# Performance work log

Hardware: AMD Instinct MI355X
Metric: run time of the kernel (lower is better)

Reference implementation:

```python
import jax, jax.numpy as jnp
import numpy as np
from jax import lax

B, N = 8, 4096
NPOINT, RADIUS, NSAMPLE = 1024, 0.2, 32
MLP = [64, 64, 128]
FEAT = 64
ALPHA = 0.2          # LeakyReLU slope
BN_EPS = 1e-5        # BatchNorm eps (eval mode, running_mean=0, running_var=1)
BIG = 1e10


def setup_inputs() -> dict:
    key = jax.random.key(0)
    ks = jax.random.split(key, 16)
    xyz = jax.random.uniform(ks[0], (B, N, 3), dtype=jnp.float32)
    feats = jax.random.normal(ks[1], (B, N, FEAT), dtype=jnp.float32)
    d = {"points": jnp.concatenate([xyz, feats], axis=-1)}
    ch = [FEAT] + MLP
    for i in range(len(MLP)):
        d[f"W{i}"] = jax.random.normal(ks[2 + 3 * i], (ch[i + 1], ch[i]), dtype=jnp.float32) * 0.1
        d[f"b{i}"] = jnp.zeros((ch[i + 1],), jnp.float32)
        d[f"g{i}"] = jnp.ones((ch[i + 1],), jnp.float32)
        d[f"be{i}"] = jnp.zeros((ch[i + 1],), jnp.float32)
    d["a_att"] = jax.random.uniform(ks[12], (3 + MLP[-1], MLP[-1]), jnp.float32, -0.3, 0.3)
    return d


def _gather(points, idx):
    # points: [B, N, D], idx: [B, ...] -> [B, ..., D]
    return jax.vmap(lambda p, i: p[i])(points, idx)


def farthest_point_sample(xyz, npoint):
    # xyz: [B, N, 3] -> [B, npoint] (deterministic start at index 0)
    b, n, _ = xyz.shape
    def step(carry, _):
        distance, farthest = carry
        centered = jnp.take_along_axis(xyz, farthest[:, None, None], axis=1)  # [B,1,3]
        dist = jnp.sum((xyz - centered) ** 2, axis=-1)                        # [B,N]
        distance = jnp.minimum(distance, dist)
        return (distance, jnp.argmax(distance, axis=-1)), farthest
    init = (jnp.full((b, n), BIG, dtype=xyz.dtype), jnp.zeros((b,), dtype=jnp.int32))
    _, idxs = lax.scan(step, init, None, length=npoint)
    return jnp.transpose(idxs)  # [B, npoint]


def query_ball_point(nsample, radius, xyz, centered_xyz):
    # squared distances [B, npoint, N]
    d = (-2.0 * jnp.einsum('bpc,bnc->bpn', centered_xyz, xyz)
         + jnp.sum(centered_xyz ** 2, -1)[..., None]
         + jnp.sum(xyz ** 2, -1)[:, None, :])
    d = jnp.where(d > radius ** 2, BIG, d)
    order = jnp.argsort(d, axis=-1)[..., :nsample]                    # [B,np,ns]
    sv = jnp.take_along_axis(d, order, axis=-1)                       # sorted values
    first = order[..., 0:1]
    return jnp.where(sv == BIG, first, order)


def _mlp(x, params):
    # x: [..., C]; 1x1 conv + BN(eval, mean=0, var=1) + relu per layer
    for (W, b, g, be) in params:
        x = jnp.einsum('...c,oc->...o', x, W) + b
        x = x * (g / jnp.sqrt(1.0 + BN_EPS)) + be
        x = jax.nn.relu(x)
    return x


def reference(points, W0, b0, g0, be0, W1, b1, g1, be1, W2, b2, g2, be2, a_att):
    xyz = points[..., :3]
    feats = points[..., 3:]
    cidx = farthest_point_sample(xyz, NPOINT)          # [B, npoint]
    cxyz = _gather(xyz, cidx)                          # [B, npoint, 3]
    cfeat = _gather(feats, cidx)                       # [B, npoint, D]
    gidx = query_ball_point(NSAMPLE, RADIUS, xyz, cxyz)  # [B, npoint, nsample]
    gxyz = _gather(xyz, gidx)                          # [B, npoint, ns, 3]
    gfeat = _gather(feats, gidx)                       # [B, npoint, ns, D]

    params = [(W0, b0, g0, be0), (W1, b1, g1, be1), (W2, b2, g2, be2)]
    cfeat = _mlp(cfeat, params)                        # [B, npoint, D']
    gfeat = _mlp(gfeat, params)                        # [B, npoint, ns, D']

    cpts = jnp.concatenate([cxyz, cfeat], axis=-1)     # [B, npoint, 3+D']
    gpts = jnp.concatenate([gxyz, gfeat], axis=-1)     # [B, npoint, ns, 3+D']

    delta = gpts - cpts[:, :, None, :]
    att = jax.nn.leaky_relu(jnp.einsum('bpnc,cd->bpnd', delta, a_att), ALPHA)
    att = jax.nn.softmax(att, axis=2)                  # over nsample (eval: no dropout)
    gac = jnp.sum(att * gfeat, axis=2)                 # [B, npoint, D']
    return jnp.concatenate([cxyz, gac], axis=-1)       # [B, npoint, 3+D']
```

## Files before the change

### kernel.cpp

```cpp
#include <hip/hip_runtime.h>
#include <math.h>

#define NBATCH 8
#define NPTS 4096
#define NPOINT 1024
#define NSAMPLE 32
#define PTDIM 67
#define BIGF 1e10f

#define DPP_QUAD_XOR1 0xB1
#define DPP_QUAD_XOR2 0x4E
#define DPP_ROW_HALF_MIRROR 0x141
#define DPP_ROW_MIRROR 0x140
#define DPP_ROW_BCAST15 0x142
#define DPP_ROW_BCAST31 0x143

template <int CTRL>
__device__ inline float dpp_mov_f(float v) {
  int i = __float_as_int(v);
  return __int_as_float(__builtin_amdgcn_update_dpp(i, i, CTRL, 0xf, 0xf, false));
}
template <int CTRL>
__device__ inline unsigned dpp_mov_u(unsigned v) {
  return (unsigned)__builtin_amdgcn_update_dpp((int)v, (int)v, CTRL, 0xf, 0xf, false);
}
template <int CTRL>
__device__ inline void dpp_min2(unsigned& hi, unsigned& lo) {
  unsigned nh = dpp_mov_u<CTRL>(hi);
  unsigned nl = dpp_mov_u<CTRL>(lo);
  bool take = (nh < hi) || (nh == hi && nl < lo);
  hi = take ? nh : hi;
  lo = take ? nl : lo;
}
__device__ inline unsigned fmap(float d) {
  unsigned b = __float_as_uint(d);
  return ((int)b < 0) ? ~b : (b | 0x80000000u);
}
#define FMAP_INF 0xFF800000u

__device__ inline float red32_max(float v) {
  v = fmaxf(v, dpp_mov_f<DPP_QUAD_XOR1>(v));
  v = fmaxf(v, dpp_mov_f<DPP_QUAD_XOR2>(v));
  v = fmaxf(v, dpp_mov_f<DPP_ROW_HALF_MIRROR>(v));
  v = fmaxf(v, dpp_mov_f<DPP_ROW_MIRROR>(v));
  v = fmaxf(v, __shfl_xor(v, 16));
  return v;
}
__device__ inline float red32_sum(float v) {
  v += dpp_mov_f<DPP_QUAD_XOR1>(v);
  v += dpp_mov_f<DPP_QUAD_XOR2>(v);
  v += dpp_mov_f<DPP_ROW_HALF_MIRROR>(v);
  v += dpp_mov_f<DPP_ROW_MIRROR>(v);
  v += __shfl_xor(v, 16);
  return v;
}

struct FpsS {
  unsigned long long slots[2][4];
  int cidxS[NPOINT];
  float4 C[NPTS];
};
struct MlpS {
  float w0[64 * 64], w1[64 * 64], w2[128 * 64];
  float bb0[64], ss0[64], ee0[64];
  float bb1[64], ss1[64], ee1[64];
  float bb2[128], ss2[128], ee2[128];
};
#define F1_SMEM (sizeof(MlpS) > sizeof(FpsS) ? sizeof(MlpS) : sizeof(FpsS))

__device__ void fps_body(char* smemRaw, const float* __restrict__ pts,
                         int* __restrict__ cidx, float* __restrict__ X,
                         float* __restrict__ Y, float* __restrict__ Z) {
#pragma clang fp contract(off)
  FpsS* S = (FpsS*)smemRaw;
  const int b = blockIdx.x, tid = threadIdx.x;
  const int w = tid >> 6, lane = tid & 63;
  const float* pb = pts + (size_t)b * NPTS * PTDIM;
  float2 px2[8], py2[8], pz2[8];
  float dl[16];
  #pragma unroll
  for (int k = 0; k < 16; k++) {
    int j = tid + (k << 8);
    const float* pj = pb + (size_t)j * PTDIM;
    float x = pj[0], y = pj[1], z = pj[2];
    if (k & 1) { px2[k >> 1].y = x; py2[k >> 1].y = y; pz2[k >> 1].y = z; }
    else       { px2[k >> 1].x = x; py2[k >> 1].x = y; pz2[k >> 1].x = z; }
    S->C[j] = make_float4(x, y, z, 0.0f);
    X[b * NPTS + j] = x; Y[b * NPTS + j] = y; Z[b * NPTS + j] = z;
    dl[k] = BIGF;
  }
  __syncthreads();
  int f = 0;
  float4 c0 = S->C[0];
  float cx = c0.x, cy = c0.y, cz = c0.z;
  for (int t = 0; t < NPOINT; t++) {
    if (tid == 0) S->cidxS[t] = f;
    float2 c2x = make_float2(cx, cx);
    float2 c2y = make_float2(cy, cy);
    float2 c2z = make_float2(cz, cz);
    #pragma unroll
    for (int m = 0; m < 8; m++) {
      float2 dx = px2[m] - c2x;
      float2 dy = py2[m] - c2y;
      float2 dz = pz2[m] - c2z;
      float2 d = (dx * dx + dy * dy) + dz * dz;
      dl[2 * m]     = fminf(dl[2 * m],     d.x);
      dl[2 * m + 1] = fminf(dl[2 * m + 1], d.y);
    }
    float u0 = fmaxf(dl[0], dl[1]),  u1 = fmaxf(dl[2], dl[3]);
    float u2 = fmaxf(dl[4], dl[5]),  u3 = fmaxf(dl[6], dl[7]);
    float u4 = fmaxf(dl[8], dl[9]),  u5 = fmaxf(dl[10], dl[11]);
    float u6 = fmaxf(dl[12], dl[13]), u7 = fmaxf(dl[14], dl[15]);
    float v0 = fmaxf(u0, u1), v1 = fmaxf(u2, u3);
    float v2 = fmaxf(u4, u5), v3 = fmaxf(u6, u7);
    float bv = fmaxf(fmaxf(v0, v1), fmaxf(v2, v3));
    float m = bv;
    m = fmaxf(m, dpp_mov_f<DPP_QUAD_XOR1>(m));
    m = fmaxf(m, dpp_mov_f<DPP_QUAD_XOR2>(m));
    m = fmaxf(m, dpp_mov_f<DPP_ROW_HALF_MIRROR>(m));
    m = fmaxf(m, dpp_mov_f<DPP_ROW_MIRROR>(m));
    m = fmaxf(m, dpp_mov_f<DPP_ROW_BCAST15>(m));
    m = fmaxf(m, dpp_mov_f<DPP_ROW_BCAST31>(m));
    unsigned wmaxbits = (unsigned)__builtin_amdgcn_readlane(__float_as_int(m), 63);
    unsigned c_[16];
    #pragma unroll
    for (int k = 0; k < 16; k++)
      c_[k] = (__float_as_uint(dl[k]) == wmaxbits) ? (unsigned)(tid + (k << 8)) : 0xFFFFFFFFu;
    unsigned q0 = min(c_[0], c_[1]),  q1 = min(c_[2], c_[3]);
    unsigned q2 = min(c_[4], c_[5]),  q3 = min(c_[6], c_[7]);
    unsigned q4 = min(c_[8], c_[9]),  q5 = min(c_[10], c_[11]);
    unsigned q6 = min(c_[12], c_[13]), q7 = min(c_[14], c_[15]);
    unsigned r0 = min(q0, q1), r1 = min(q2, q3), r2 = min(q4, q5), r3 = min(q6, q7);
    unsigned cand = min(min(r0, r1), min(r2, r3));
    cand = min(cand, dpp_mov_u<DPP_QUAD_XOR1>(cand));
    cand = min(cand, dpp_mov_u<DPP_QUAD_XOR2>(cand));
    cand = min(cand, dpp_mov_u<DPP_ROW_HALF_MIRROR>(cand));
    cand = min(cand, dpp_mov_u<DPP_ROW_MIRROR>(cand));
    cand = min(cand, dpp_mov_u<DPP_ROW_BCAST15>(cand));
    cand = min(cand, dpp_mov_u<DPP_ROW_BCAST31>(cand));
    unsigned jmin = (unsigned)__builtin_amdgcn_readlane((int)cand, 63);
    if (lane == 0)
      S->slots[t & 1][w] = ((unsigned long long)wmaxbits << 32) |
                           (unsigned long long)(NPTS - 1 - jmin);
    __syncthreads();
    unsigned long long s0 = S->slots[t & 1][0], s1 = S->slots[t & 1][1];
    unsigned long long s2 = S->slots[t & 1][2], s3 = S->slots[t & 1][3];
    unsigned long long m0 = s0 > s1 ? s0 : s1;
    unsigned long long m1 = s2 > s3 ? s2 : s3;
    unsigned long long best = m0 > m1 ? m0 : m1;
    f = NPTS - 1 - (int)(best & 0xFFFFFFFFull);
    float4 cc = S->C[f];
    cx = cc.x; cy = cc.y; cz = cc.z;
  }
  __syncthreads();
  for (int i = tid; i < NPOINT; i += 256) cidx[b * NPOINT + i] = S->cidxS[i];
}

__device__ void mlp_body(char* smemRaw, const float* __restrict__ pts,
    const float* __restrict__ W0, const float* __restrict__ B0, const float* __restrict__ G0, const float* __restrict__ E0,
    const float* __restrict__ W1, const float* __restrict__ B1, const float* __restrict__ G1, const float* __restrict__ E1,
    const float* __restrict__ W2, const float* __restrict__ B2, const float* __restrict__ G2, const float* __restrict__ E2,
    float* __restrict__ mfeat) {
  MlpS* S = (MlpS*)smemRaw;
  const float INVS = 0.99999500003750f;
  const int t = threadIdx.x;
  for (int i = t; i < 4096; i += 256) { S->w0[i] = W0[i]; S->w1[i] = W1[i]; }
  for (int i = t; i < 8192; i += 256) { S->w2[i] = W2[i]; }
  if (t < 64) {
    S->bb0[t] = B0[t]; S->ss0[t] = G0[t] * INVS; S->ee0[t] = E0[t];
    S->bb1[t] = B1[t]; S->ss1[t] = G1[t] * INVS; S->ee1[t] = E1[t];
  }
  if (t < 128) { S->bb2[t] = B2[t]; S->ss2[t] = G2[t] * INVS; S->ee2[t] = E2[t]; }
  __syncthreads();

  const size_t r = (size_t)(blockIdx.x - 8) * 256 + t;
  const float* xr = pts + r * PTDIM + 3;
  float x[64];
  #pragma unroll
  for (int c = 0; c < 64; c++) x[c] = xr[c];

  float h1[64];
  #pragma unroll
  for (int o = 0; o < 64; o++) {
    float acc = S->bb0[o];
    #pragma unroll
    for (int c = 0; c < 64; c += 4) {
      float4 wv = *(const float4*)&S->w0[o * 64 + c];
      acc = fmaf(wv.x, x[c], acc);
      acc = fmaf(wv.y, x[c + 1], acc);
      acc = fmaf(wv.z, x[c + 2], acc);
      acc = fmaf(wv.w, x[c + 3], acc);
    }
    h1[o] = fmaxf(fmaf(acc, S->ss0[o], S->ee0[o]), 0.0f);
  }
  float h2[64];
  #pragma unroll
  for (int o = 0; o < 64; o++) {
    float acc = S->bb1[o];
    #pragma unroll
    for (int c = 0; c < 64; c += 4) {
      float4 wv = *(const float4*)&S->w1[o * 64 + c];
      acc = fmaf(wv.x, h1[c], acc);
      acc = fmaf(wv.y, h1[c + 1], acc);
      acc = fmaf(wv.z, h1[c + 2], acc);
      acc = fmaf(wv.w, h1[c + 3], acc);
    }
    h2[o] = fmaxf(fmaf(acc, S->ss1[o], S->ee1[o]), 0.0f);
  }
  float* orow = mfeat + r * 128;
  #pragma unroll
  for (int o = 0; o < 128; o += 4) {
    float a0 = S->bb2[o], a1 = S->bb2[o + 1], a2 = S->bb2[o + 2], a3 = S->bb2[o + 3];
    #pragma unroll
    for (int c = 0; c < 64; c += 4) {
      float4 wv0 = *(const float4*)&S->w2[(o    ) * 64 + c];
      float4 wv1 = *(const float4*)&S->w2[(o + 1) * 64 + c];
      float4 wv2 = *(const float4*)&S->w2[(o + 2) * 64 + c];
      float4 wv3 = *(const float4*)&S->w2[(o + 3) * 64 + c];
      a0 = fmaf(wv0.x, h2[c], a0); a0 = fmaf(wv0.y, h2[c+1], a0); a0 = fmaf(wv0.z, h2[c+2], a0); a0 = fmaf(wv0.w, h2[c+3], a0);
      a1 = fmaf(wv1.x, h2[c], a1); a1 = fmaf(wv1.y, h2[c+1], a1); a1 = fmaf(wv1.z, h2[c+2], a1); a1 = fmaf(wv1.w, h2[c+3], a1);
      a2 = fmaf(wv2.x, h2[c], a2); a2 = fmaf(wv2.y, h2[c+1], a2); a2 = fmaf(wv2.z, h2[c+2], a2); a2 = fmaf(wv2.w, h2[c+3], a2);
      a3 = fmaf(wv3.x, h2[c], a3); a3 = fmaf(wv3.y, h2[c+1], a3); a3 = fmaf(wv3.z, h2[c+2], a3); a3 = fmaf(wv3.w, h2[c+3], a3);
    }
    float4 ov;
    ov.x = fmaxf(fmaf(a0, S->ss2[o    ], S->ee2[o    ]), 0.0f);
    ov.y = fmaxf(fmaf(a1, S->ss2[o + 1], S->ee2[o + 1]), 0.0f);
    ov.z = fmaxf(fmaf(a2, S->ss2[o + 2], S->ee2[o + 2]), 0.0f);
    ov.w = fmaxf(fmaf(a3, S->ss2[o + 3], S->ee2[o + 3]), 0.0f);
    *(float4*)(orow + o) = ov;
  }
}

__global__ __launch_bounds__(256) void f1_kernel(const float* __restrict__ pts,
    const float* __restrict__ W0, const float* __restrict__ B0, const float* __restrict__ G0, const float* __restrict__ E0,
    const float* __restrict__ W1, const float* __restrict__ B1, const float* __restrict__ G1, const float* __restrict__ E1,
    const float* __restrict__ W2, const float* __restrict__ B2, const float* __restrict__ G2, const float* __restrict__ E2,
    float* __restrict__ mfeat, int* __restrict__ cidx,
    float* __restrict__ X, float* __restrict__ Y, float* __restrict__ Z) {
  __shared__ __align__(16) char smem[F1_SMEM];
  if (blockIdx.x < 8)
    fps_body(smem, pts, cidx, X, Y, Z);
  else
    mlp_body(smem, pts, W0, B0, G0, E0, W1, B1, G1, E1, W2, B2, G2, E2, mfeat);
}

#define F2_SMEM 16768

__device__ void ballq_body(char* smemRaw,
                           const float* __restrict__ X, const float* __restrict__ Y,
                           const float* __restrict__ Z, const int* __restrict__ cidx,
                           int* __restrict__ gidx) {
  float (*dbuf)[512] = (float (*)[512])smemRaw;
  int   (*ibuf)[512] = (int (*)[512])(smemRaw + 4 * 512 * 4);
  const int t = threadIdx.x;
  const int w = t >> 6, lane = t & 63;
  const int pc = blockIdx.x * 4 + w;
  const int b = pc >> 10;
  const float* Xb = X + b * NPTS;
  const float* Yb = Y + b * NPTS;
  const float* Zb = Z + b * NPTS;
  const int cI = cidx[pc];
  const float cx = Xb[cI], cy = Yb[cI], cz = Zb[cI];
  const float sc = __fadd_rn(__fadd_rn(__fmul_rn(cx, cx), __fmul_rn(cy, cy)), __fmul_rn(cz, cz));
  const float R2 = 0.04f;
  int cnt = 0;
  for (int rr = 0; rr < 16; rr++) {
    const int base = rr * 256 + lane * 4;
    float4 px4 = *(const float4*)(Xb + base);
    float4 py4 = *(const float4*)(Yb + base);
    float4 pz4 = *(const float4*)(Zb + base);
    #pragma unroll
    for (int e = 0; e < 4; e++) {
      float px = e == 0 ? px4.x : e == 1 ? px4.y : e == 2 ? px4.z : px4.w;
      float py = e == 0 ? py4.x : e == 1 ? py4.y : e == 2 ? py4.z : py4.w;
      float pz = e == 0 ? pz4.x : e == 1 ? pz4.y : e == 2 ? pz4.z : pz4.w;
      float dot = __fadd_rn(__fadd_rn(__fmul_rn(cx, px), __fmul_rn(cy, py)), __fmul_rn(cz, pz));
      float sx  = __fadd_rn(__fadd_rn(__fmul_rn(px, px), __fmul_rn(py, py)), __fmul_rn(pz, pz));
      float d   = __fadd_rn(__fadd_rn(__fmul_rn(-2.0f, dot), sc), sx);
      bool pred = !(d > R2);
      unsigned long long mask = __ballot(pred);
      if (pred) {
        int pos = cnt + (int)__popcll(mask & ((1ull << lane) - 1ull));
        if (pos < 512) { dbuf[w][pos] = d; ibuf[w][pos] = base + e; }
      }
      cnt += (int)__popcll(mask);
    }
  }
  const int K = cnt < 512 ? cnt : 512;
  unsigned long long kk[8];
  #pragma unroll
  for (int k = 0; k < 8; k++) {
    int pos = lane + 64 * k;
    if (pos < K)
      kk[k] = ((unsigned long long)fmap(dbuf[w][pos]) << 32) | (unsigned)ibuf[w][pos];
    else
      kk[k] = ((unsigned long long)FMAP_INF << 32) | 0x7fffffffu;
  }
  int first = 0;
  int* gout = gidx + pc * NSAMPLE;
  for (int it = 0; it < NSAMPLE; it++) {
    unsigned long long best = kk[0];
    #pragma unroll
    for (int k = 1; k < 8; k++) if (kk[k] < best) best = kk[k];
    unsigned hi = (unsigned)(best >> 32), lo = (unsigned)best;
    dpp_min2<DPP_QUAD_XOR1>(hi, lo);
    dpp_min2<DPP_QUAD_XOR2>(hi, lo);
    dpp_min2<DPP_ROW_HALF_MIRROR>(hi, lo);
    dpp_min2<DPP_ROW_MIRROR>(hi, lo);
    dpp_min2<DPP_ROW_BCAST15>(hi, lo);
    dpp_min2<DPP_ROW_BCAST31>(hi, lo);
    unsigned blo = (unsigned)__builtin_amdgcn_readlane((int)lo, 63);
    #pragma unroll
    for (int k = 0; k < 8; k++)
      if ((unsigned)kk[k] == blo)
        kk[k] = (kk[k] & 0xFFFFFFFFull) | ((unsigned long long)FMAP_INF << 32);
    if (it == 0) first = (int)blo;
    if (lane == 0) gout[it] = (it < K) ? (int)blo : first;
  }
}

__device__ void proj_body(char* smemRaw,
                          const float* __restrict__ X, const float* __restrict__ Y,
                          const float* __restrict__ Z, const float* __restrict__ mfeat,
                          const float* __restrict__ Aatt, float* __restrict__ P) {
  float* As = (float*)smemRaw;
  const int t = threadIdx.x;
  const int pb = blockIdx.x - 2048;
  const int grp = pb & 3;
  const int tile = pb >> 2;
  for (int i = t; i < 131 * 32; i += 256) {
    int c = i >> 5, col = i & 31;
    As[i] = Aatt[c * 128 + grp * 32 + col];
  }
  __syncthreads();
  const int r0 = tile * 512 + t * 2;
  float acc0[32], acc1[32];
  {
    float x0 = X[r0], y0 = Y[r0], z0 = Z[r0];
    float x1 = X[r0 + 1], y1 = Y[r0 + 1], z1 = Z[r0 + 1];
    #pragma unroll
    for (int j = 0; j < 32; j += 4) {
      float4 a0 = *(const float4*)&As[0 * 32 + j];
      float4 a1 = *(const float4*)&As[1 * 32 + j];
      float4 a2 = *(const float4*)&As[2 * 32 + j];
      acc0[j]   = fmaf(z0, a2.x, fmaf(y0, a1.x, x0 * a0.x));
      acc0[j+1] = fmaf(z0, a2.y, fmaf(y0, a1.y, x0 * a0.y));
      acc0[j+2] = fmaf(z0, a2.z, fmaf(y0, a1.z, x0 * a0.z));
      acc0[j+3] = fmaf(z0, a2.w, fmaf(y0, a1.w, x0 * a0.w));
      acc1[j]   = fmaf(z1, a2.x, fmaf(y1, a1.x, x1 * a0.x));
      acc1[j+1] = fmaf(z1, a2.y, fmaf(y1, a1.y, x1 * a0.y));
      acc1[j+2] = fmaf(z1, a2.z, fmaf(y1, a1.z, x1 * a0.z));
      acc1[j+3] = fmaf(z1, a2.w, fmaf(y1, a1.w, x1 * a0.w));
    }
  }
  const float* m0 = mfeat + (size_t)r0 * 128;
  const float* m1 = m0 + 128;
  for (int c = 0; c < 128; c += 4) {
    float4 v0 = *(const float4*)(m0 + c);
    float4 v1 = *(const float4*)(m1 + c);
    #pragma unroll
    for (int u = 0; u < 4; u++) {
      const float* arow = &As[(3 + c + u) * 32];
      float s0 = u == 0 ? v0.x : u == 1 ? v0.y : u == 2 ? v0.z : v0.w;
      float s1 = u == 0 ? v1.x : u == 1 ? v1.y : u == 2 ? v1.z : v1.w;
      #pragma unroll
      for (int j = 0; j < 32; j += 4) {
        float4 a = *(const float4*)&arow[j];
        acc0[j]   = fmaf(s0, a.x, acc0[j]);
        acc0[j+1] = fmaf(s0, a.y, acc0[j+1]);
        acc0[j+2] = fmaf(s0, a.z, acc0[j+2]);
        acc0[j+3] = fmaf(s0, a.w, acc0[j+3]);
        acc1[j]   = fmaf(s1, a.x, acc1[j]);
        acc1[j+1] = fmaf(s1, a.y, acc1[j+1]);
        acc1[j+2] = fmaf(s1, a.z, acc1[j+2]);
        acc1[j+3] = fmaf(s1, a.w, acc1[j+3]);
      }
    }
  }
  float* p0 = P + (size_t)r0 * 128 + grp * 32;
  float* p1 = p0 + 128;
  #pragma unroll
  for (int j = 0; j < 32; j += 4) {
    *(float4*)(p0 + j) = make_float4(acc0[j], acc0[j+1], acc0[j+2], acc0[j+3]);
    *(float4*)(p1 + j) = make_float4(acc1[j], acc1[j+1], acc1[j+2], acc1[j+3]);
  }
}

__global__ __launch_bounds__(256) void f2_kernel(
    const float* __restrict__ X, const float* __restrict__ Y, const float* __restrict__ Z,
    const int* __restrict__ cidx, int* __restrict__ gidx,
    const float* __restrict__ mfeat, const float* __restrict__ Aatt,
    float* __restrict__ P) {
  __shared__ __align__(16) char smem[F2_SMEM];
  if (blockIdx.x < 2048)
    ballq_body(smem, X, Y, Z, cidx, gidx);
  else
    proj_body(smem, X, Y, Z, mfeat, Aatt, P);
}

__global__ __launch_bounds__(256) void attn_kernel(
    const float* __restrict__ X, const float* __restrict__ Y, const float* __restrict__ Z,
    const float* __restrict__ mfeat, const float* __restrict__ P,
    const int* __restrict__ cidx, const int* __restrict__ gidx,
    float* __restrict__ out) {
  __shared__ float pcS[128];
  const int pc = (blockIdx.x & 7) * 1024 + (blockIdx.x >> 3);
  const int b = pc >> 10;
  const int t = threadIdx.x;
  const int n = t & 31, q = t >> 5;
  const int cI = cidx[pc];
  if (t < 128) pcS[t] = P[((size_t)b * NPTS + cI) * 128 + t];
  const int g = gidx[pc * NSAMPLE + n];
  const float* Pg = P + ((size_t)b * NPTS + g) * 128 + q * 16;
  const float* Gf = mfeat + ((size_t)b * NPTS + g) * 128 + q * 16;
  __syncthreads();
  float a[16], gfv[16];
  #pragma unroll
  for (int k = 0; k < 4; k++) {
    float4 vg = *(const float4*)(Pg + 4 * k);
    float4 vc = *(const float4*)&pcS[q * 16 + 4 * k];
    float4 vf = *(const float4*)(Gf + 4 * k);
    a[4*k]   = vg.x - vc.x; a[4*k+1] = vg.y - vc.y;
    a[4*k+2] = vg.z - vc.z; a[4*k+3] = vg.w - vc.w;
    gfv[4*k] = vf.x; gfv[4*k+1] = vf.y; gfv[4*k+2] = vf.z; gfv[4*k+3] = vf.w;
  }
  #pragma unroll
  for (int j = 0; j < 16; j++) a[j] = a[j] >= 0.0f ? a[j] : 0.2f * a[j];
  float e[16], s[16], num[16];
  #pragma unroll
  for (int j = 0; j < 16; j++) {
    float mx = red32_max(a[j]);
    e[j] = expf(a[j] - mx);
  }
  #pragma unroll
  for (int j = 0; j < 16; j++) s[j] = red32_sum(e[j]);
  #pragma unroll
  for (int j = 0; j < 16; j++) num[j] = red32_sum(e[j] * gfv[j]);
  if (n == 0) {
    float* orow = out + (size_t)pc * 131;
    #pragma unroll
    for (int j = 0; j < 16; j++) orow[3 + q * 16 + j] = num[j] / s[j];
    if (q == 0) {
      orow[0] = X[b * NPTS + cI]; orow[1] = Y[b * NPTS + cI]; orow[2] = Z[b * NPTS + cI];
    }
  }
}

extern "C" void kernel_launch(void* const* d_in, const int* in_sizes, int n_in,
                              void* d_out, int out_size, void* d_ws, size_t ws_size,
                              hipStream_t stream) {
  const float* points = (const float*)d_in[0];
  const float* W0 = (const float*)d_in[1];
  const float* B0 = (const float*)d_in[2];
  const float* G0 = (const float*)d_in[3];
  const float* E0 = (const float*)d_in[4];
  const float* W1 = (const float*)d_in[5];
  const float* B1 = (const float*)d_in[6];
  const float* G1 = (const float*)d_in[7];
  const float* E1 = (const float*)d_in[8];
  const float* W2 = (const float*)d_in[9];
  const float* B2 = (const float*)d_in[10];
  const float* G2 = (const float*)d_in[11];
  const float* E2 = (const float*)d_in[12];
  const float* Aatt = (const float*)d_in[13];
  float* out = (float*)d_out;

  float* mfeat = (float*)d_ws;
  float* Pw = mfeat + (size_t)NBATCH * NPTS * 128;
  float* Xw = Pw + (size_t)NBATCH * NPTS * 128;
  float* Yw = Xw + NBATCH * NPTS;
  float* Zw = Yw + NBATCH * NPTS;
  int* cidxw = (int*)(Zw + NBATCH * NPTS);
  int* gidxw = cidxw + NBATCH * NPOINT;

  f1_kernel<<<8 + NBATCH * NPTS / 256, 256, 0, stream>>>(points,
      W0, B0, G0, E0, W1, B1, G1, E1, W2, B2, G2, E2, mfeat, cidxw, Xw, Yw, Zw);
  f2_kernel<<<2048 + 256, 256, 0, stream>>>(Xw, Yw, Zw, cidxw, gidxw, mfeat, Aatt, Pw);
  attn_kernel<<<NBATCH * NPOINT, 256, 0, stream>>>(Xw, Yw, Zw, mfeat, Pw, cidxw, gidxw, out);
}
```

Measured before the change: 864.6 us.

## Fuse attention projection into MLP blocks so it overlaps farthest-point sampling

The attention-weight projection P moves out of the second kernel and into the MLP blocks of the first kernel. Each MLP block now handles 512 rows and projects each row's 128-dim output right after computing it, with the full attention matrix held in shared memory. This removes the mfeat re-read and the extra projection blocks from the ball-query kernel, and the projection now runs in the shadow of the serial FPS blocks. In exchange, the first kernel uses much more LDS per block (about 131KB) and more registers, and runs far fewer MLP blocks.

```diff
diff --git a/kernel.cpp b/kernel.cpp
--- a/kernel.cpp
+++ b/kernel.cpp
@@ -60,13 +60,14 @@
   int cidxS[NPOINT];
   float4 C[NPTS];
 };
-struct MlpS {
+struct ProjS {
+  float As[131 * 128];
   float w0[64 * 64], w1[64 * 64], w2[128 * 64];
   float bb0[64], ss0[64], ee0[64];
   float bb1[64], ss1[64], ee1[64];
   float bb2[128], ss2[128], ee2[128];
 };
-#define F1_SMEM (sizeof(MlpS) > sizeof(FpsS) ? sizeof(MlpS) : sizeof(FpsS))
+#define F1_SMEM (sizeof(ProjS) > sizeof(FpsS) ? sizeof(ProjS) : sizeof(FpsS))
 
 __device__ void fps_body(char* smemRaw, const float* __restrict__ pts,
                          int* __restrict__ cidx, float* __restrict__ X,
@@ -156,16 +157,18 @@
   for (int i = tid; i < NPOINT; i += 256) cidx[b * NPOINT + i] = S->cidxS[i];
 }
 
-__device__ void mlp_body(char* smemRaw, const float* __restrict__ pts,
+__device__ void projmlp_body(char* smemRaw, const float* __restrict__ pts,
     const float* __restrict__ W0, const float* __restrict__ B0, const float* __restrict__ G0, const float* __restrict__ E0,
     const float* __restrict__ W1, const float* __restrict__ B1, const float* __restrict__ G1, const float* __restrict__ E1,
     const float* __restrict__ W2, const float* __restrict__ B2, const float* __restrict__ G2, const float* __restrict__ E2,
-    float* __restrict__ mfeat) {
-  MlpS* S = (MlpS*)smemRaw;
+    const float* __restrict__ Aatt,
+    float* __restrict__ mfeat, float* __restrict__ P) {
+  ProjS* S = (ProjS*)smemRaw;
   const float INVS = 0.99999500003750f;
   const int t = threadIdx.x;
+  for (int i = t; i < 131 * 128; i += 256) S->As[i] = Aatt[i];
   for (int i = t; i < 4096; i += 256) { S->w0[i] = W0[i]; S->w1[i] = W1[i]; }
-  for (int i = t; i < 8192; i += 256) { S->w2[i] = W2[i]; }
+  for (int i = t; i < 8192; i += 256) S->w2[i] = W2[i];
   if (t < 64) {
     S->bb0[t] = B0[t]; S->ss0[t] = G0[t] * INVS; S->ee0[t] = E0[t];
     S->bb1[t] = B1[t]; S->ss1[t] = G1[t] * INVS; S->ee1[t] = E1[t];
@@ -173,61 +176,96 @@
   if (t < 128) { S->bb2[t] = B2[t]; S->ss2[t] = G2[t] * INVS; S->ee2[t] = E2[t]; }
   __syncthreads();
 
-  const size_t r = (size_t)(blockIdx.x - 8) * 256 + t;
-  const float* xr = pts + r * PTDIM + 3;
-  float x[64];
-  #pragma unroll
-  for (int c = 0; c < 64; c++) x[c] = xr[c];
-
-  float h1[64];
-  #pragma unroll
-  for (int o = 0; o < 64; o++) {
-    float acc = S->bb0[o];
-    #pragma unroll
-    for (int c = 0; c < 64; c += 4) {
-      float4 wv = *(const float4*)&S->w0[o * 64 + c];
-      acc = fmaf(wv.x, x[c], acc);
-      acc = fmaf(wv.y, x[c + 1], acc);
-      acc = fmaf(wv.z, x[c + 2], acc);
-      acc = fmaf(wv.w, x[c + 3], acc);
-    }
-    h1[o] = fmaxf(fmaf(acc, S->ss0[o], S->ee0[o]), 0.0f);
-  }
-  float h2[64];
-  #pragma unroll
-  for (int o = 0; o < 64; o++) {
-    float acc = S->bb1[o];
-    #pragma unroll
-    for (int c = 0; c < 64; c += 4) {
-      float4 wv = *(const float4*)&S->w1[o * 64 + c];
-      acc = fmaf(wv.x, h1[c], acc);
-      acc = fmaf(wv.y, h1[c + 1], acc);
-      acc = fmaf(wv.z, h1[c + 2], acc);
-      acc = fmaf(wv.w, h1[c + 3], acc);
-    }
-    h2[o] = fmaxf(fmaf(acc, S->ss1[o], S->ee1[o]), 0.0f);
-  }
-  float* orow = mfeat + r * 128;
-  #pragma unroll
-  for (int o = 0; o < 128; o += 4) {
-    float a0 = S->bb2[o], a1 = S->bb2[o + 1], a2 = S->bb2[o + 2], a3 = S->bb2[o + 3];
-    #pragma unroll
-    for (int c = 0; c < 64; c += 4) {
-      float4 wv0 = *(const float4*)&S->w2[(o    ) * 64 + c];
-      float4 wv1 = *(const float4*)&S->w2[(o + 1) * 64 + c];
-      float4 wv2 = *(const float4*)&S->w2[(o + 2) * 64 + c];
-      float4 wv3 = *(const float4*)&S->w2[(o + 3) * 64 + c];
-      a0 = fmaf(wv0.x, h2[c], a0); a0 = fmaf(wv0.y, h2[c+1], a0); a0 = fmaf(wv0.z, h2[c+2], a0); a0 = fmaf(wv0.w, h2[c+3], a0);
-      a1 = fmaf(wv1.x, h2[c], a1); a1 = fmaf(wv1.y, h2[c+1], a1); a1 = fmaf(wv1.z, h2[c+2], a1); a1 = fmaf(wv1.w, h2[c+3], a1);
-      a2 = fmaf(wv2.x, h2[c], a2); a2 = fmaf(wv2.y, h2[c+1], a2); a2 = fmaf(wv2.z, h2[c+2], a2); a2 = fmaf(wv2.w, h2[c+3], a2);
-      a3 = fmaf(wv3.x, h2[c], a3); a3 = fmaf(wv3.y, h2[c+1], a3); a3 = fmaf(wv3.z, h2[c+2], a3); a3 = fmaf(wv3.w, h2[c+3], a3);
-    }
-    float4 ov;
-    ov.x = fmaxf(fmaf(a0, S->ss2[o    ], S->ee2[o    ]), 0.0f);
-    ov.y = fmaxf(fmaf(a1, S->ss2[o + 1], S->ee2[o + 1]), 0.0f);
-    ov.z = fmaxf(fmaf(a2, S->ss2[o + 2], S->ee2[o + 2]), 0.0f);
-    ov.w = fmaxf(fmaf(a3, S->ss2[o + 3], S->ee2[o + 3]), 0.0f);
-    *(float4*)(orow + o) = ov;
+  const int pb = blockIdx.x - 8;
+  for (int rr = 0; rr < 2; rr++) {
+    const size_t r = (size_t)pb * 512 + rr * 256 + t;
+    const float* xr = pts + r * PTDIM + 3;
+    float x[64];
+    #pragma unroll
+    for (int c = 0; c < 64; c++) x[c] = xr[c];
+
+    float h1[64];
+    #pragma unroll
+    for (int o = 0; o < 64; o++) {
+      float acc = S->bb0[o];
+      #pragma unroll
+      for (int c = 0; c < 64; c += 4) {
+        float4 wv = *(const float4*)&S->w0[o * 64 + c];
+        acc = fmaf(wv.x, x[c], acc);
+        acc = fmaf(wv.y, x[c + 1], acc);
+        acc = fmaf(wv.z, x[c + 2], acc);
+        acc = fmaf(wv.w, x[c + 3], acc);
+      }
+      h1[o] = fmaxf(fmaf(acc, S->ss0[o], S->ee0[o]), 0.0f);
+    }
+    float h2[64];
+    #pragma unroll
+    for (int o = 0; o < 64; o++) {
+      float acc = S->bb1[o];
+      #pragma unroll
+      for (int c = 0; c < 64; c += 4) {
+        float4 wv = *(const float4*)&S->w1[o * 64 + c];
+        acc = fmaf(wv.x, h1[c], acc);
+        acc = fmaf(wv.y, h1[c + 1], acc);
+        acc = fmaf(wv.z, h1[c + 2], acc);
+        acc = fmaf(wv.w, h1[c + 3], acc);
+      }
+      h2[o] = fmaxf(fmaf(acc, S->ss1[o], S->ee1[o]), 0.0f);
+    }
+    float h3[128];
+    float* orow = mfeat + r * 128;
+    #pragma unroll
+    for (int o = 0; o < 128; o += 4) {
+      float a0 = S->bb2[o], a1 = S->bb2[o + 1], a2 = S->bb2[o + 2], a3 = S->bb2[o + 3];
+      #pragma unroll
+      for (int c = 0; c < 64; c += 4) {
+        float4 wv0 = *(const float4*)&S->w2[(o    ) * 64 + c];
+        float4 wv1 = *(const float4*)&S->w2[(o + 1) * 64 + c];
+        float4 wv2 = *(const float4*)&S->w2[(o + 2) * 64 + c];
+        float4 wv3 = *(const float4*)&S->w2[(o + 3) * 64 + c];
+        a0 = fmaf(wv0.x, h2[c], a0); a0 = fmaf(wv0.y, h2[c+1], a0); a0 = fmaf(wv0.z, h2[c+2], a0); a0 = fmaf(wv0.w, h2[c+3], a0);
+        a1 = fmaf(wv1.x, h2[c], a1); a1 = fmaf(wv1.y, h2[c+1], a1); a1 = fmaf(wv1.z, h2[c+2], a1); a1 = fmaf(wv1.w, h2[c+3], a1);
+        a2 = fmaf(wv2.x, h2[c], a2); a2 = fmaf(wv2.y, h2[c+1], a2); a2 = fmaf(wv2.z, h2[c+2], a2); a2 = fmaf(wv2.w, h2[c+3], a2);
+        a3 = fmaf(wv3.x, h2[c], a3); a3 = fmaf(wv3.y, h2[c+1], a3); a3 = fmaf(wv3.z, h2[c+2], a3); a3 = fmaf(wv3.w, h2[c+3], a3);
+      }
+      float4 ov;
+      ov.x = fmaxf(fmaf(a0, S->ss2[o    ], S->ee2[o    ]), 0.0f);
+      ov.y = fmaxf(fmaf(a1, S->ss2[o + 1], S->ee2[o + 1]), 0.0f);
+      ov.z = fmaxf(fmaf(a2, S->ss2[o + 2], S->ee2[o + 2]), 0.0f);
+      ov.w = fmaxf(fmaf(a3, S->ss2[o + 3], S->ee2[o + 3]), 0.0f);
+      h3[o] = ov.x; h3[o + 1] = ov.y; h3[o + 2] = ov.z; h3[o + 3] = ov.w;
+      *(float4*)(orow + o) = ov;
+    }
+    const float* pr = pts + r * PTDIM;
+    float x0 = pr[0], y0 = pr[1], z0 = pr[2];
+    float* prow = P + r * 128;
+    for (int grp = 0; grp < 4; grp++) {
+      const int g0 = grp * 32;
+      float acc[32];
+      #pragma unroll
+      for (int j = 0; j < 32; j++) {
+        float a0 = S->As[0 * 128 + g0 + j];
+        float a1 = S->As[1 * 128 + g0 + j];
+        float a2 = S->As[2 * 128 + g0 + j];
+        acc[j] = fmaf(z0, a2, fmaf(y0, a1, x0 * a0));
+      }
+      #pragma unroll
+      for (int c = 0; c < 128; c++) {
+        float s = h3[c];
+        const float* arow = &S->As[(3 + c) * 128 + g0];
+        #pragma unroll
+        for (int j = 0; j < 32; j += 4) {
+          float4 a = *(const float4*)&arow[j];
+          acc[j]   = fmaf(s, a.x, acc[j]);
+          acc[j+1] = fmaf(s, a.y, acc[j+1]);
+          acc[j+2] = fmaf(s, a.z, acc[j+2]);
+          acc[j+3] = fmaf(s, a.w, acc[j+3]);
+        }
+      }
+      #pragma unroll
+      for (int j = 0; j < 32; j += 4)
+        *(float4*)(prow + g0 + j) = make_float4(acc[j], acc[j+1], acc[j+2], acc[j+3]);
+    }
   }
 }
 
@@ -235,23 +273,22 @@
     const float* __restrict__ W0, const float* __restrict__ B0, const float* __restrict__ G0, const float* __restrict__ E0,
     const float* __restrict__ W1, const float* __restrict__ B1, const float* __restrict__ G1, const float* __restrict__ E1,
     const float* __restrict__ W2, const float* __restrict__ B2, const float* __restrict__ G2, const float* __restrict__ E2,
-    float* __restrict__ mfeat, int* __restrict__ cidx,
+    const float* __restrict__ Aatt,
+    float* __restrict__ mfeat, float* __restrict__ P, int* __restrict__ cidx,
     float* __restrict__ X, float* __restrict__ Y, float* __restrict__ Z) {
   __shared__ __align__(16) char smem[F1_SMEM];
   if (blockIdx.x < 8)
     fps_body(smem, pts, cidx, X, Y, Z);
   else
-    mlp_body(smem, pts, W0, B0, G0, E0, W1, B1, G1, E1, W2, B2, G2, E2, mfeat);
-}
-
-#define F2_SMEM 16768
-
-__device__ void ballq_body(char* smemRaw,
-                           const float* __restrict__ X, const float* __restrict__ Y,
-                           const float* __restrict__ Z, const int* __restrict__ cidx,
-                           int* __restrict__ gidx) {
-  float (*dbuf)[512] = (float (*)[512])smemRaw;
-  int   (*ibuf)[512] = (int (*)[512])(smemRaw + 4 * 512 * 4);
+    projmlp_body(smem, pts, W0, B0, G0, E0, W1, B1, G1, E1, W2, B2, G2, E2,
+                 Aatt, mfeat, P);
+}
+
+__global__ __launch_bounds__(256) void f2_kernel(
+    const float* __restrict__ X, const float* __restrict__ Y, const float* __restrict__ Z,
+    const int* __restrict__ cidx, int* __restrict__ gidx) {
+  __shared__ float dbuf[4][512];
+  __shared__ int   ibuf[4][512];
   const int t = threadIdx.x;
   const int w = t >> 6, lane = t & 63;
   const int pc = blockIdx.x * 4 + w;
@@ -317,85 +354,6 @@
     if (it == 0) first = (int)blo;
     if (lane == 0) gout[it] = (it < K) ? (int)blo : first;
   }
-}
-
-__device__ void proj_body(char* smemRaw,
-                          const float* __restrict__ X, const float* __restrict__ Y,
-                          const float* __restrict__ Z, const float* __restrict__ mfeat,
-                          const float* __restrict__ Aatt, float* __restrict__ P) {
-  float* As = (float*)smemRaw;
-  const int t = threadIdx.x;
-  const int pb = blockIdx.x - 2048;
-  const int grp = pb & 3;
-  const int tile = pb >> 2;
-  for (int i = t; i < 131 * 32; i += 256) {
-    int c = i >> 5, col = i & 31;
-    As[i] = Aatt[c * 128 + grp * 32 + col];
-  }
-  __syncthreads();
-  const int r0 = tile * 512 + t * 2;
-  float acc0[32], acc1[32];
-  {
-    float x0 = X[r0], y0 = Y[r0], z0 = Z[r0];
-    float x1 = X[r0 + 1], y1 = Y[r0 + 1], z1 = Z[r0 + 1];
-    #pragma unroll
-    for (int j = 0; j < 32; j += 4) {
-      float4 a0 = *(const float4*)&As[0 * 32 + j];
-      float4 a1 = *(const float4*)&As[1 * 32 + j];
-      float4 a2 = *(const float4*)&As[2 * 32 + j];
-      acc0[j]   = fmaf(z0, a2.x, fmaf(y0, a1.x, x0 * a0.x));
-      acc0[j+1] = fmaf(z0, a2.y, fmaf(y0, a1.y, x0 * a0.y));
-      acc0[j+2] = fmaf(z0, a2.z, fmaf(y0, a1.z, x0 * a0.z));
-      acc0[j+3] = fmaf(z0, a2.w, fmaf(y0, a1.w, x0 * a0.w));
-      acc1[j]   = fmaf(z1, a2.x, fmaf(y1, a1.x, x1 * a0.x));
-      acc1[j+1] = fmaf(z1, a2.y, fmaf(y1, a1.y, x1 * a0.y));
-      acc1[j+2] = fmaf(z1, a2.z, fmaf(y1, a1.z, x1 * a0.z));
-      acc1[j+3] = fmaf(z1, a2.w, fmaf(y1, a1.w, x1 * a0.w));
-    }
-  }
-  const float* m0 = mfeat + (size_t)r0 * 128;
-  const float* m1 = m0 + 128;
-  for (int c = 0; c < 128; c += 4) {
-    float4 v0 = *(const float4*)(m0 + c);
-    float4 v1 = *(const float4*)(m1 + c);
-    #pragma unroll
-    for (int u = 0; u < 4; u++) {
-      const float* arow = &As[(3 + c + u) * 32];
-      float s0 = u == 0 ? v0.x : u == 1 ? v0.y : u == 2 ? v0.z : v0.w;
-      float s1 = u == 0 ? v1.x : u == 1 ? v1.y : u == 2 ? v1.z : v1.w;
-      #pragma unroll
-      for (int j = 0; j < 32; j += 4) {
-        float4 a = *(const float4*)&arow[j];
-        acc0[j]   = fmaf(s0, a.x, acc0[j]);
-        acc0[j+1] = fmaf(s0, a.y, acc0[j+1]);
-        acc0[j+2] = fmaf(s0, a.z, acc0[j+2]);
-        acc0[j+3] = fmaf(s0, a.w, acc0[j+3]);
-        acc1[j]   = fmaf(s1, a.x, acc1[j]);
-        acc1[j+1] = fmaf(s1, a.y, acc1[j+1]);
-        acc1[j+2] = fmaf(s1, a.z, acc1[j+2]);
-        acc1[j+3] = fmaf(s1, a.w, acc1[j+3]);
-      }
-    }
-  }
-  float* p0 = P + (size_t)r0 * 128 + grp * 32;
-  float* p1 = p0 + 128;
-  #pragma unroll
-  for (int j = 0; j < 32; j += 4) {
-    *(float4*)(p0 + j) = make_float4(acc0[j], acc0[j+1], acc0[j+2], acc0[j+3]);
-    *(float4*)(p1 + j) = make_float4(acc1[j], acc1[j+1], acc1[j+2], acc1[j+3]);
-  }
-}
-
-__global__ __launch_bounds__(256) void f2_kernel(
-    const float* __restrict__ X, const float* __restrict__ Y, const float* __restrict__ Z,
-    const int* __restrict__ cidx, int* __restrict__ gidx,
-    const float* __restrict__ mfeat, const float* __restrict__ Aatt,
-    float* __restrict__ P) {
-  __shared__ __align__(16) char smem[F2_SMEM];
-  if (blockIdx.x < 2048)
-    ballq_body(smem, X, Y, Z, cidx, gidx);
-  else
-    proj_body(smem, X, Y, Z, mfeat, Aatt, P);
 }
 
 __global__ __launch_bounds__(256) void attn_kernel(
@@ -473,8 +431,9 @@
   int* cidxw = (int*)(Zw + NBATCH * NPTS);
   int* gidxw = cidxw + NBATCH * NPOINT;
 
-  f1_kernel<<<8 + NBATCH * NPTS / 256, 256, 0, stream>>>(points,
-      W0, B0, G0, E0, W1, B1, G1, E1, W2, B2, G2, E2, mfeat, cidxw, Xw, Yw, Zw);
-  f2_kernel<<<2048 + 256, 256, 0, stream>>>(Xw, Yw, Zw, cidxw, gidxw, mfeat, Aatt, Pw);
+  f1_kernel<<<8 + 64, 256, 0, stream>>>(points,
+      W0, B0, G0, E0, W1, B1, G1, E1, W2, B2, G2, E2, Aatt,
+      mfeat, Pw, cidxw, Xw, Yw, Zw);
+  f2_kernel<<<NBATCH * NPOINT / 4, 256, 0, stream>>>(Xw, Yw, Zw, cidxw, gidxw);
   attn_kernel<<<NBATCH * NPOINT, 256, 0, stream>>>(Xw, Yw, Zw, mfeat, Pw, cidxw, gidxw, out);
 }
```

Result: faster. 833.5 us (-3.6%).
